# Kernel tuning notes

Hardware: AMD Instinct MI355X
Metric: run time of the kernel (lower is better)

## Reference

```python
import jax, jax.numpy as jnp
import numpy as np

N_NODES = 100000
N_EDGES = 1600000
NFEAT = 256
NCLASS = 2


def setup_inputs() -> dict:
    key = jax.random.key(0)
    ks = jax.random.split(key, 16)
    x = jax.random.normal(ks[0], (N_NODES, NFEAT), dtype=jnp.float32)
    row = jax.random.randint(ks[1], (N_EDGES,), 0, N_NODES, dtype=jnp.int64) if jax.config.jax_enable_x64 else jax.random.randint(ks[1], (N_EDGES,), 0, N_NODES, dtype=jnp.int32)
    col = jax.random.randint(ks[2], (N_EDGES,), 0, N_NODES, dtype=row.dtype)
    edge_val = jax.random.uniform(ks[3], (N_EDGES,), dtype=jnp.float32)

    def unif(k, shape, fan_out):
        stdv = 1.0 / np.sqrt(fan_out)
        return jax.random.uniform(k, shape, dtype=jnp.float32, minval=-stdv, maxval=stdv)

    W1 = unif(ks[4], (NFEAT, 32), 32); b1 = unif(ks[5], (32,), 32)
    W2 = unif(ks[6], (32, 48), 48);   b2 = unif(ks[7], (48,), 48)
    W3 = unif(ks[8], (48, 64), 64);   b3 = unif(ks[9], (64,), 64)
    fc1_W = unif(ks[10], (64, 32), 64); fc1_b = unif(ks[11], (32,), 64)
    fc2_W = unif(ks[12], (32, NCLASS), 32); fc2_b = unif(ks[13], (NCLASS,), 32)
    return {"x": x, "row": row, "col": col, "edge_val": edge_val,
            "W1": W1, "b1": b1, "W2": W2, "b2": b2, "W3": W3, "b3": b3,
            "fc1_W": fc1_W, "fc1_b": fc1_b, "fc2_W": fc2_W, "fc2_b": fc2_b}


def _spmm(row, col, val, dense):
    # out[i] = sum_{e: row[e]==i} val[e] * dense[col[e]]   (COO sparse @ dense)
    gathered = dense[col] * val[:, None]          # [E, F]
    return jax.ops.segment_sum(gathered, row, num_segments=N_NODES)


def _gc_layer(x, row, col, val, W, b):
    support = x @ W                               # dense mm  [N, out]
    return _spmm(row, col, val, support) + b      # spmm + bias


def reference(x, row, col, edge_val, W1, b1, W2, b2, W3, b3, fc1_W, fc1_b, fc2_W, fc2_b):
    # eval mode: dropout is identity
    h = jax.nn.relu(_gc_layer(x, row, col, edge_val, W1, b1))   # [N, 32]
    h = jax.nn.relu(_gc_layer(h, row, col, edge_val, W2, b2))   # [N, 48]
    h = jax.nn.relu(_gc_layer(h, row, col, edge_val, W3, b3))   # [N, 64]
    y = jnp.mean(h, axis=0)                                     # [64] global mean pool
    y = jax.nn.relu(y @ fc1_W + fc1_b)                          # [32]
    y = jax.nn.softmax(y @ fc2_W + fc2_b, axis=0)               # [nclass]
    return y
```

## Files before the change

kernel.cpp:

```cpp
#include <hip/hip_runtime.h>
#include <hip/hip_bf16.h>

#define N_NODES 100000
#define N_EDGES 1600000

#define NT 391
#define NB1 128
#define CHUNK ((N_EDGES + NB1 - 1) / NB1)
#define ROWS3 40
#define GRID3 (N_NODES / ROWS3)
#define GB1 ((N_NODES + 63) / 64)

__device__ __forceinline__ unsigned char f2q(float f) {
    return (unsigned char)(__builtin_amdgcn_cvt_pk_fp8_f32(f, f, 0, false) & 0xFF);
}
__device__ __forceinline__ unsigned pack4_fp8(float a0, float a1, float a2, float a3) {
    int r = __builtin_amdgcn_cvt_pk_fp8_f32(a0, a1, 0, false);
    r = __builtin_amdgcn_cvt_pk_fp8_f32(a2, a3, r, true);
    return (unsigned)r;
}
#define CVT(u, s) __builtin_amdgcn_cvt_f32_fp8((u), (s))

#define ACC4(A, U, V)                                                               \
    A[0] += (V) * CVT((U), 0); A[1] += (V) * CVT((U), 1);                           \
    A[2] += (V) * CVT((U), 2); A[3] += (V) * CVT((U), 3);

#define ACC8(A, U, V)                                                               \
    A[0] += (V) * CVT((U).x, 0); A[1] += (V) * CVT((U).x, 1);                       \
    A[2] += (V) * CVT((U).x, 2); A[3] += (V) * CVT((U).x, 3);                       \
    A[4] += (V) * CVT((U).y, 0); A[5] += (V) * CVT((U).y, 1);                       \
    A[6] += (V) * CVT((U).y, 2); A[7] += (V) * CVT((U).y, 3);

__global__ __launch_bounds__(256) void k_gemm1_phist(const float* __restrict__ x, const float* __restrict__ W,
                                                     unsigned char* __restrict__ out,
                                                     const int* __restrict__ row, int* __restrict__ blkhist) {
    __shared__ __align__(16) char smem[64 * 65 * 4];
    int tid = threadIdx.x;
    if (blockIdx.x >= GB1) {
        int* h = (int*)smem;
        int b = blockIdx.x - GB1;
        for (int i = tid; i < NT; i += 256) h[i] = 0;
        __syncthreads();
        int s = b * CHUNK, e = min(s + CHUNK, N_EDGES);
        for (int i = s + tid; i < e; i += 256) atomicAdd(&h[row[i] >> 8], 1);
        __syncthreads();
        for (int i = tid; i < NT; i += 256) blkhist[i * NB1 + b] = h[i];
        return;
    }
    float (*xsT)[65] = (float(*)[65])smem;
    int bn = blockIdx.x * 64;
    int lane = tid & 63;
    int o8 = __builtin_amdgcn_readfirstlane(tid >> 6) * 8;
    const float* Wp = W + o8;
    float acc[8] = {};
    for (int kc = 0; kc < 4; ++kc) {
        int k0 = kc * 64;
        __syncthreads();
        #pragma unroll
        for (int i = 0; i < 4; ++i) {
            int idx = i * 256 + tid;
            int n = idx >> 4;
            int k4 = (idx & 15) * 4;
            float4 v = make_float4(0.f, 0.f, 0.f, 0.f);
            if (bn + n < N_NODES)
                v = *reinterpret_cast<const float4*>(&x[(size_t)(bn + n) * 256 + k0 + k4]);
            xsT[k4 + 0][n] = v.x; xsT[k4 + 1][n] = v.y; xsT[k4 + 2][n] = v.z; xsT[k4 + 3][n] = v.w;
        }
        __syncthreads();
        #pragma unroll 8
        for (int k = 0; k < 64; ++k) {
            float xv = xsT[k][lane];
            const float* wr = Wp + (size_t)(k0 + k) * 32;
            float4 wa = *reinterpret_cast<const float4*>(wr);
            float4 wb = *reinterpret_cast<const float4*>(wr + 4);
            acc[0] += xv * wa.x; acc[1] += xv * wa.y; acc[2] += xv * wa.z; acc[3] += xv * wa.w;
            acc[4] += xv * wb.x; acc[5] += xv * wb.y; acc[6] += xv * wb.z; acc[7] += xv * wb.w;
        }
    }
    int n = bn + lane;
    if (n < N_NODES) {
        uint2 r;
        r.x = pack4_fp8(acc[0], acc[1], acc[2], acc[3]);
        r.y = pack4_fp8(acc[4], acc[5], acc[6], acc[7]);
        *reinterpret_cast<uint2*>(&out[(size_t)n * 32 + o8]) = r;
    }
}


__global__ __launch_bounds__(128) void k_bscan1(int* __restrict__ blkhist, int* __restrict__ cnt) {
    __shared__ int s[128];
    int j = blockIdx.x, t = threadIdx.x;
    int v = blkhist[j * NB1 + t];
    s[t] = v;
    __syncthreads();
    #pragma unroll
    for (int st = 1; st < 128; st <<= 1) {
        int u = (t >= st) ? s[t - st] : 0;
        __syncthreads();
        s[t] += u;
        __syncthreads();
    }
    blkhist[j * NB1 + t] = s[t] - v;
    if (t == 127) cnt[j] = s[127];
}

__global__ __launch_bounds__(512) void k_bscan2(const int* __restrict__ cnt, int* __restrict__ base,
                                                int* __restrict__ row_ptr) {
    __shared__ int s[512];
    int j = threadIdx.x;
    int v = (j < NT) ? cnt[j] : 0;
    s[j] = v;
    __syncthreads();
    for (int st = 1; st < 512; st <<= 1) {
        int u = (j >= st) ? s[j - st] : 0;
        __syncthreads();
        s[j] += u;
        __syncthreads();
    }
    if (j < NT) base[j] = s[j] - v;
    if (j == 0) row_ptr[N_NODES] = N_EDGES;
}

__global__ __launch_bounds__(256) void k_pscatter(const int* __restrict__ row, const int* __restrict__ col,
                                                  const float* __restrict__ val,
                                                  const int* __restrict__ blkhist, const int* __restrict__ base,
                                                  int2* __restrict__ part) {
    __shared__ int cur[NT];
    int b = blockIdx.x, t = threadIdx.x;
    for (int i = t; i < NT; i += 256) cur[i] = blkhist[i * NB1 + b] + base[i];
    __syncthreads();
    int s = b * CHUNK, e = min(s + CHUNK, N_EDGES);
    for (int i = s + t; i < e; i += 256) {
        int r = row[i];
        int j = r >> 8;
        int p = atomicAdd(&cur[j], 1);
        part[p] = make_int2(((r & 255) << 24) | col[i], __float_as_int(val[i]));
    }
}

__global__ __launch_bounds__(256) void k_sort(const int2* __restrict__ part, const int* __restrict__ cnt,
                                              const int* __restrict__ base, int* __restrict__ row_ptr,
                                              unsigned* __restrict__ csr) {
    __shared__ int hist[256];
    __shared__ int cur[256];
    int b = blockIdx.x, t = threadIdx.x;
    int n = cnt[b];
    int bb = base[b];
    const int2* sl = part + bb;
    hist[t] = 0;
    __syncthreads();
    for (int i = t; i < n; i += 256) atomicAdd(&hist[((unsigned)sl[i].x) >> 24], 1);
    __syncthreads();
    int v = hist[t];
    for (int st = 1; st < 256; st <<= 1) {
        int u = (t >= st) ? hist[t - st] : 0;
        __syncthreads();
        hist[t] += u;
        __syncthreads();
    }
    cur[t] = hist[t] - v;
    int grow = b * 256 + t;
    if (grow < N_NODES) row_ptr[grow] = bb + cur[t];
    __syncthreads();
    for (int i = t; i < n; i += 256) {
        int2 e = sl[i];
        int rl = ((unsigned)e.x) >> 24;
        int p = atomicAdd(&cur[rl], 1);
        unsigned c = (unsigned)(e.x & 0xFFFFFF);
        float vf = __int_as_float(e.y);
        int q = __float2int_rn(vf * 32768.0f);
        if (q > 32767) q = 32767;
        csr[bb + p] = (c << 15) | (unsigned)q;
    }
}

__global__ __launch_bounds__(256, 8) void k_spmm1(const int* __restrict__ rp, const unsigned* __restrict__ csr,
                                                  const unsigned char* __restrict__ sup,
                                                  const float* __restrict__ bias,
                                                  unsigned char* __restrict__ out) {
    int gid = blockIdx.x * 256 + threadIdx.x;
    int n = gid >> 3;
    if (n >= N_NODES) return;
    int f4 = (gid & 7) * 4;
    int e0 = rp[n], e1 = rp[n + 1];
    float a[4] = {};
    int e = e0;
    if ((e & 1) && e < e1) {
        unsigned ent = csr[e];
        float v = (float)(ent & 0x7FFF);
        unsigned u = *reinterpret_cast<const unsigned*>(&sup[(size_t)(ent >> 15) * 32 + f4]);
        ACC4(a, u, v)
        ++e;
    }
    for (; e + 1 < e1; e += 2) {
        uint2 p = *reinterpret_cast<const uint2*>(&csr[e]);
        unsigned u0 = *reinterpret_cast<const unsigned*>(&sup[(size_t)(p.x >> 15) * 32 + f4]);
        unsigned u1 = *reinterpret_cast<const unsigned*>(&sup[(size_t)(p.y >> 15) * 32 + f4]);
        float v0 = (float)(p.x & 0x7FFF), v1 = (float)(p.y & 0x7FFF);
        ACC4(a, u0, v0)
        ACC4(a, u1, v1)
    }
    if (e < e1) {
        unsigned ent = csr[e];
        float v = (float)(ent & 0x7FFF);
        unsigned u = *reinterpret_cast<const unsigned*>(&sup[(size_t)(ent >> 15) * 32 + f4]);
        ACC4(a, u, v)
    }
    const float sc = 1.0f / 32768.0f;
    unsigned r = pack4_fp8(fmaxf(a[0] * sc + bias[f4 + 0], 0.f), fmaxf(a[1] * sc + bias[f4 + 1], 0.f),
                           fmaxf(a[2] * sc + bias[f4 + 2], 0.f), fmaxf(a[3] * sc + bias[f4 + 3], 0.f));
    *reinterpret_cast<unsigned*>(&out[(size_t)n * 32 + f4]) = r;
}

__global__ __launch_bounds__(256, 8) void k_l2fused(const int* __restrict__ rp, const unsigned* __restrict__ csr,
                                                    const unsigned char* __restrict__ h1,
                                                    const float* __restrict__ W2, const float* __restrict__ b2,
                                                    unsigned char* __restrict__ h2) {
    __shared__ float w2s[32 * 48];
    __shared__ float b2s[48];
    __shared__ float g2s[32][33];
    int tid = threadIdx.x;
    for (int i = tid; i < 32 * 48; i += 256) w2s[i] = W2[i];
    if (tid < 48) b2s[tid] = b2[tid];
    int n0 = blockIdx.x * 32;
    int grp = tid >> 3;
    int f4 = (tid & 7) * 4;
    int n = n0 + grp;
    {
        int e0 = rp[n], e1 = rp[n + 1];
        float a[4] = {};
        int e = e0;
        if ((e & 1) && e < e1) {
            unsigned ent = csr[e];
            float v = (float)(ent & 0x7FFF);
            unsigned u = *reinterpret_cast<const unsigned*>(&h1[(size_t)(ent >> 15) * 32 + f4]);
            ACC4(a, u, v)
            ++e;
        }
        for (; e + 1 < e1; e += 2) {
            uint2 p = *reinterpret_cast<const uint2*>(&csr[e]);
            unsigned u0 = *reinterpret_cast<const unsigned*>(&h1[(size_t)(p.x >> 15) * 32 + f4]);
            unsigned u1 = *reinterpret_cast<const unsigned*>(&h1[(size_t)(p.y >> 15) * 32 + f4]);
            float v0 = (float)(p.x & 0x7FFF), v1 = (float)(p.y & 0x7FFF);
            ACC4(a, u0, v0)
            ACC4(a, u1, v1)
        }
        if (e < e1) {
            unsigned ent = csr[e];
            float v = (float)(ent & 0x7FFF);
            unsigned u = *reinterpret_cast<const unsigned*>(&h1[(size_t)(ent >> 15) * 32 + f4]);
            ACC4(a, u, v)
        }
        const float sc = 1.0f / 32768.0f;
        g2s[grp][f4 + 0] = a[0] * sc;
        g2s[grp][f4 + 1] = a[1] * sc;
        g2s[grp][f4 + 2] = a[2] * sc;
        g2s[grp][f4 + 3] = a[3] * sc;
    }
    __syncthreads();
    #pragma unroll
    for (int pp = 0; pp < 6; ++pp) {
        int idx = pp * 256 + tid;
        int r = idx / 48;
        int m = idx - 48 * r;
        float a = b2s[m];
        const float* g = g2s[r];
        #pragma unroll
        for (int k = 0; k < 32; ++k) a += g[k] * w2s[k * 48 + m];
        h2[(size_t)(n0 + r) * 48 + m] = f2q(fmaxf(a, 0.f));
    }
}

__global__ __launch_bounds__(256, 7) void k_l3fused(const int* __restrict__ rp, const unsigned* __restrict__ csr,
                                                    const unsigned char* __restrict__ h2,
                                                    const float* __restrict__ W3, const float* __restrict__ b3,
                                                    float* __restrict__ poolpart) {
    __shared__ float w3s[48 * 64];
    __shared__ float b3s[64];
    __shared__ float g3s[ROWS3][49];
    __shared__ float red[256];
    int tid = threadIdx.x;
    for (int i = tid; i < 48 * 64; i += 256) w3s[i] = W3[i];
    if (tid < 64) b3s[tid] = b3[tid];
    int grp = tid / 6;
    int f8 = (tid - grp * 6) * 8;
    int m = tid & 63;
    const float sc = 1.0f / 32768.0f;
    if (tid < 240) {
        int n = blockIdx.x * ROWS3 + grp;
        int e0 = rp[n], e1 = rp[n + 1];
        float a[8] = {};
        int e = e0;
        if ((e & 1) && e < e1) {
            unsigned ent = csr[e];
            float v = (float)(ent & 0x7FFF);
            uint2 u = *reinterpret_cast<const uint2*>(&h2[(size_t)(ent >> 15) * 48 + f8]);
            ACC8(a, u, v)
            ++e;
        }
        for (; e + 1 < e1; e += 2) {
            uint2 p = *reinterpret_cast<const uint2*>(&csr[e]);
            uint2 u0 = *reinterpret_cast<const uint2*>(&h2[(size_t)(p.x >> 15) * 48 + f8]);
            uint2 u1 = *reinterpret_cast<const uint2*>(&h2[(size_t)(p.y >> 15) * 48 + f8]);
            float v0 = (float)(p.x & 0x7FFF), v1 = (float)(p.y & 0x7FFF);
            ACC8(a, u0, v0)
            ACC8(a, u1, v1)
        }
        if (e < e1) {
            unsigned ent = csr[e];
            float v = (float)(ent & 0x7FFF);
            uint2 u = *reinterpret_cast<const uint2*>(&h2[(size_t)(ent >> 15) * 48 + f8]);
            ACC8(a, u, v)
        }
        #pragma unroll
        for (int j = 0; j < 8; ++j) g3s[grp][f8 + j] = a[j] * sc;
    }
    __syncthreads();
    float poolacc = 0.f;
    #pragma unroll
    for (int pp = 0; pp < 10; ++pp) {
        int r = 4 * pp + (tid >> 6);
        float a = b3s[m];
        const float* gg = g3s[r];
        #pragma unroll
        for (int k = 0; k < 48; ++k) a += gg[k] * w3s[k * 64 + m];
        poolacc += fmaxf(a, 0.f);
    }
    red[tid] = poolacc;
    __syncthreads();
    if (tid < 64) {
        float s = red[tid] + red[tid + 64] + red[tid + 128] + red[tid + 192];
        poolpart[(size_t)blockIdx.x * 64 + tid] = s;
    }
}

__global__ __launch_bounds__(256) void k_preduce(const float* __restrict__ poolpart,
                                                 float* __restrict__ pool) {
    __shared__ float red[256];
    int b = blockIdx.x, t = threadIdx.x;
    float s = 0.f;
    for (int j = t; j < GRID3; j += 256) s += poolpart[(size_t)j * 64 + b];
    red[t] = s;
    __syncthreads();
    for (int st = 128; st > 0; st >>= 1) {
        if (t < st) red[t] += red[t + st];
        __syncthreads();
    }
    if (t == 0) pool[b] = red[0];
}

__global__ __launch_bounds__(64) void k_head(const float* __restrict__ pool,
                                             const float* __restrict__ fc1W, const float* __restrict__ fc1b,
                                             const float* __restrict__ fc2W, const float* __restrict__ fc2b,
                                             float* __restrict__ out) {
    __shared__ float pl[64];
    __shared__ float z[32];
    __shared__ float lg[2];
    int t = threadIdx.x;
    pl[t] = pool[t] * (1.0f / (float)N_NODES);
    __syncthreads();
    if (t < 32) {
        float a = fc1b[t];
        #pragma unroll
        for (int o = 0; o < 64; ++o) a += pl[o] * fc1W[o * 32 + t];
        z[t] = fmaxf(a, 0.f);
    }
    __syncthreads();
    if (t < 2) {
        float l = fc2b[t];
        #pragma unroll
        for (int j = 0; j < 32; ++j) l += z[j] * fc2W[j * 2 + t];
        lg[t] = l;
    }
    __syncthreads();
    if (t == 0) {
        float mx = fmaxf(lg[0], lg[1]);
        float e0 = __expf(lg[0] - mx), e1 = __expf(lg[1] - mx);
        float ss = e0 + e1;
        out[0] = e0 / ss;
        out[1] = e1 / ss;
    }
}


extern "C" void kernel_launch(void* const* d_in, const int* in_sizes, int n_in,
                              void* d_out, int out_size, void* d_ws, size_t ws_size,
                              hipStream_t stream) {
    const float* x    = (const float*)d_in[0];
    const int*   row  = (const int*)d_in[1];
    const int*   col  = (const int*)d_in[2];
    const float* val  = (const float*)d_in[3];
    const float* W1   = (const float*)d_in[4];
    const float* b1   = (const float*)d_in[5];
    const float* W2   = (const float*)d_in[6];
    const float* b2   = (const float*)d_in[7];
    const float* W3   = (const float*)d_in[8];
    const float* b3   = (const float*)d_in[9];
    const float* fc1W = (const float*)d_in[10];
    const float* fc1b = (const float*)d_in[11];
    const float* fc2W = (const float*)d_in[12];
    const float* fc2b = (const float*)d_in[13];
    float* out = (float*)d_out;

    char* wsb = (char*)d_ws;
    size_t off = 0;
    auto alloc = [&](size_t bytes) {
        void* p = wsb + off;
        off += (bytes + 255) / 256 * 256;
        return p;
    };
    int*      blkhist  = (int*)alloc((size_t)NT * NB1 * 4);
    int*      base     = (int*)alloc((size_t)NT * 4);
    int*      cnt      = (int*)alloc((size_t)NT * 4);
    int*      row_ptr  = (int*)alloc((size_t)(N_NODES + 1) * 4);
    int2*     part     = (int2*)alloc((size_t)N_EDGES * 8);
    unsigned* csr      = (unsigned*)alloc((size_t)N_EDGES * 4);
    unsigned char* sup = (unsigned char*)alloc((size_t)N_NODES * 32);
    unsigned char* h1  = (unsigned char*)alloc((size_t)N_NODES * 32);
    unsigned char* h2  = (unsigned char*)alloc((size_t)N_NODES * 48);
    float* poolpart    = (float*)alloc((size_t)GRID3 * 64 * 4);
    float* pool        = (float*)alloc(64 * 4);

    k_gemm1_phist<<<GB1 + NB1, 256, 0, stream>>>(x, W1, sup, row, blkhist);
    k_bscan1<<<NT, 128, 0, stream>>>(blkhist, cnt);
    k_bscan2<<<1, 512, 0, stream>>>(cnt, base, row_ptr);
    k_pscatter<<<NB1, 256, 0, stream>>>(row, col, val, blkhist, base, part);
    k_sort<<<NT, 256, 0, stream>>>(part, cnt, base, row_ptr, csr);

    k_spmm1<<<(N_NODES * 8 + 255) / 256, 256, 0, stream>>>(row_ptr, csr, sup, b1, h1);
    k_l2fused<<<(N_NODES + 31) / 32, 256, 0, stream>>>(row_ptr, csr, h1, W2, b2, h2);
    k_l3fused<<<GRID3, 256, 0, stream>>>(row_ptr, csr, h2, W3, b3, poolpart);
    k_preduce<<<64, 256, 0, stream>>>(poolpart, pool);
    k_head<<<1, 64, 0, stream>>>(pool, fc1W, fc1b, fc2W, fc2b, out);
}
```

Baseline: 217.9 us.

## Compute full 32-wide GEMM1 row per thread without LDS staging

```diff
diff --git a/kernel.cpp b/kernel.cpp
--- a/kernel.cpp
+++ b/kernel.cpp
@@ -9,7 +9,7 @@
 #define CHUNK ((N_EDGES + NB1 - 1) / NB1)
 #define ROWS3 40
 #define GRID3 (N_NODES / ROWS3)
-#define GB1 ((N_NODES + 63) / 64)
+#define GB1 ((N_NODES + 255) / 256)
 
 __device__ __forceinline__ unsigned char f2q(float f) {
     return (unsigned char)(__builtin_amdgcn_cvt_pk_fp8_f32(f, f, 0, false) & 0xFF);
@@ -34,10 +34,9 @@
 __global__ __launch_bounds__(256) void k_gemm1_phist(const float* __restrict__ x, const float* __restrict__ W,
                                                      unsigned char* __restrict__ out,
                                                      const int* __restrict__ row, int* __restrict__ blkhist) {
-    __shared__ __align__(16) char smem[64 * 65 * 4];
+    __shared__ int h[NT];
     int tid = threadIdx.x;
     if (blockIdx.x >= GB1) {
-        int* h = (int*)smem;
         int b = blockIdx.x - GB1;
         for (int i = tid; i < NT; i += 256) h[i] = 0;
         __syncthreads();
@@ -47,43 +46,32 @@
         for (int i = tid; i < NT; i += 256) blkhist[i * NB1 + b] = h[i];
         return;
     }
-    float (*xsT)[65] = (float(*)[65])smem;
-    int bn = blockIdx.x * 64;
-    int lane = tid & 63;
-    int o8 = __builtin_amdgcn_readfirstlane(tid >> 6) * 8;
-    const float* Wp = W + o8;
-    float acc[8] = {};
-    for (int kc = 0; kc < 4; ++kc) {
-        int k0 = kc * 64;
-        __syncthreads();
-        #pragma unroll
-        for (int i = 0; i < 4; ++i) {
-            int idx = i * 256 + tid;
-            int n = idx >> 4;
-            int k4 = (idx & 15) * 4;
-            float4 v = make_float4(0.f, 0.f, 0.f, 0.f);
-            if (bn + n < N_NODES)
-                v = *reinterpret_cast<const float4*>(&x[(size_t)(bn + n) * 256 + k0 + k4]);
-            xsT[k4 + 0][n] = v.x; xsT[k4 + 1][n] = v.y; xsT[k4 + 2][n] = v.z; xsT[k4 + 3][n] = v.w;
-        }
-        __syncthreads();
-        #pragma unroll 8
-        for (int k = 0; k < 64; ++k) {
-            float xv = xsT[k][lane];
-            const float* wr = Wp + (size_t)(k0 + k) * 32;
-            float4 wa = *reinterpret_cast<const float4*>(wr);
-            float4 wb = *reinterpret_cast<const float4*>(wr + 4);
-            acc[0] += xv * wa.x; acc[1] += xv * wa.y; acc[2] += xv * wa.z; acc[3] += xv * wa.w;
-            acc[4] += xv * wb.x; acc[5] += xv * wb.y; acc[6] += xv * wb.z; acc[7] += xv * wb.w;
-        }
-    }
-    int n = bn + lane;
-    if (n < N_NODES) {
-        uint2 r;
-        r.x = pack4_fp8(acc[0], acc[1], acc[2], acc[3]);
-        r.y = pack4_fp8(acc[4], acc[5], acc[6], acc[7]);
-        *reinterpret_cast<uint2*>(&out[(size_t)n * 32 + o8]) = r;
-    }
+    int n = blockIdx.x * 256 + tid;
+    if (n >= N_NODES) return;
+    const float* xr = x + (size_t)n * 256;
+    float acc[32] = {};
+    for (int kc = 0; kc < 64; ++kc) {
+        float4 xv = *reinterpret_cast<const float4*>(xr + kc * 4);
+        const float* wr = W + kc * 128;
+        #pragma unroll
+        for (int m = 0; m < 32; ++m) {
+            acc[m] += xv.x * wr[m];
+            acc[m] += xv.y * wr[32 + m];
+            acc[m] += xv.z * wr[64 + m];
+            acc[m] += xv.w * wr[96 + m];
+        }
+    }
+    uint4 r0, r1;
+    r0.x = pack4_fp8(acc[0],  acc[1],  acc[2],  acc[3]);
+    r0.y = pack4_fp8(acc[4],  acc[5],  acc[6],  acc[7]);
+    r0.z = pack4_fp8(acc[8],  acc[9],  acc[10], acc[11]);
+    r0.w = pack4_fp8(acc[12], acc[13], acc[14], acc[15]);
+    r1.x = pack4_fp8(acc[16], acc[17], acc[18], acc[19]);
+    r1.y = pack4_fp8(acc[20], acc[21], acc[22], acc[23]);
+    r1.z = pack4_fp8(acc[24], acc[25], acc[26], acc[27]);
+    r1.w = pack4_fp8(acc[28], acc[29], acc[30], acc[31]);
+    *reinterpret_cast<uint4*>(&out[(size_t)n * 32 + 0])  = r0;
+    *reinterpret_cast<uint4*>(&out[(size_t)n * 32 + 16]) = r1;
 }
 
 
```

Measured after the change: 229.9 us. 5.5% more time.
